# Kernel optimization log

Measured on AMD Instinct MI355X. Metric: run time of the kernel, lower is better.

The kernel has to match this reference:

```python
import jax, jax.numpy as jnp
import numpy as np

D_MODEL, D_STATE, EXPAND = 1024, 16, 2
D_INNER = D_MODEL * EXPAND
BATCH, SEQ = 4, 2048
DT = 0.1

def setup_inputs() -> dict:
    key = jax.random.key(0)
    ks = jax.random.split(key, 12)
    s = 0.02
    inp = {
        "x": jax.random.normal(ks[0], (BATCH, SEQ, D_MODEL), jnp.float32),
        "B_mod": jax.random.normal(ks[1], (BATCH, D_STATE), jnp.float32) * 0.1,
        "C_mod": jax.random.normal(ks[2], (BATCH, D_STATE), jnp.float32) * 0.1,
        "W_in": jax.random.normal(ks[3], (D_MODEL, 2 * D_INNER), jnp.float32) * s,
        "b_in": jnp.zeros((2 * D_INNER,), jnp.float32),
        "conv_w": jax.random.normal(ks[4], (D_INNER, 1, 3), jnp.float32) * 0.3,
        "conv_b": jnp.zeros((D_INNER,), jnp.float32),
        "A_log": jnp.tile(jnp.log(jnp.arange(1, D_STATE + 1, dtype=jnp.float32))[None, :], (D_INNER, 1)),
        "D": jnp.ones((D_INNER,), jnp.float32),
        "W_B": jax.random.normal(ks[5], (D_INNER, D_STATE), jnp.float32) * s,
        "b_B": jnp.zeros((D_STATE,), jnp.float32),
        "W_C": jax.random.normal(ks[6], (D_INNER, D_STATE), jnp.float32) * s,
        "b_C": jnp.zeros((D_STATE,), jnp.float32),
        "W_out": jax.random.normal(ks[7], (D_INNER, D_MODEL), jnp.float32) * s,
        "b_out": jnp.zeros((D_MODEL,), jnp.float32),
    }
    return inp

def _silu(v):
    return v * jax.nn.sigmoid(v)

def reference(x, B_mod, C_mod, W_in, b_in, conv_w, conv_b, A_log, D, W_B, b_B, W_C, b_C, W_out, b_out):
    # in_proj + split + gate
    xr = x @ W_in + b_in                      # (B, L, 2*D_INNER)
    x_ssm, x_res = jnp.split(xr, 2, axis=-1)
    x_ssm = _silu(x_ssm)
    # depthwise conv1d, kernel 3, padding 1
    xc = jnp.transpose(x_ssm, (0, 2, 1))      # (B, C, L)
    xc = jax.lax.conv_general_dilated(
        xc, conv_w, window_strides=(1,), padding=[(1, 1)],
        dimension_numbers=("NCH", "OIH", "NCH"), feature_group_count=D_INNER)
    xc = xc + conv_b[None, :, None]
    x_ssm = jnp.transpose(xc, (0, 2, 1))      # (B, L, D_INNER)
    # SSM params
    A = -jnp.exp(A_log)                       # (D_INNER, D_STATE)
    A_bar = jnp.exp(A * DT)
    B = x_ssm @ W_B + b_B + B_mod[:, None, :] # (B, L, D_STATE)
    C = x_ssm @ W_C + b_C + C_mod[:, None, :]
    # sequential scan over time
    def step(h, inp):
        xt, Bt, Ct = inp                      # (B,D_INNER), (B,S), (B,S)
        h = A_bar[None] * h + xt[:, :, None] * Bt[:, None, :]
        yt = jnp.einsum("bds,bs->bd", h, Ct)
        return h, yt
    h0 = jnp.zeros((x.shape[0], D_INNER, D_STATE), x.dtype)
    xs = (jnp.moveaxis(x_ssm, 1, 0), jnp.moveaxis(B, 1, 0), jnp.moveaxis(C, 1, 0))
    _, ys = jax.lax.scan(step, h0, xs)        # (L, B, D_INNER)
    y = jnp.moveaxis(ys, 0, 1) + D[None, None, :] * x_ssm
    y = y * _silu(x_res)
    return y @ W_out + b_out
```

## Files before the change

### kernel.cpp

```cpp
#include <hip/hip_runtime.h>
#include <stdint.h>

#define D_MODEL 1024
#define D_STATE 16
#define D_INNER 2048
#define BATCH   4
#define SEQ     2048
#define ML      (BATCH*SEQ)
#define CH      64
#define NCHUNK  (SEQ/CH)
#define KSEG    8

typedef unsigned short u16;
typedef u16   u16x8  __attribute__((ext_vector_type(8)));
typedef short s16x8  __attribute__((ext_vector_type(8)));
typedef float f32x4  __attribute__((ext_vector_type(4)));

__device__ __forceinline__ float b2f(u16 u){
  union { uint32_t i; float f; } v; v.i = ((uint32_t)u) << 16; return v.f;
}
__device__ __forceinline__ u16 f2b(float f){
  uint32_t x = __float_as_uint(f);
  return (u16)((x + 0x7fffu + ((x >> 16) & 1u)) >> 16);
}
__device__ __forceinline__ float silu_f(float v){
  return v / (1.f + __expf(-v));
}
__device__ __forceinline__ void gl_lds16(const void* gp, void* lp){
  __builtin_amdgcn_global_load_lds(
      (const __attribute__((address_space(1))) void*)gp,
      (__attribute__((address_space(3))) void*)lp, 16, 0, 0);
}

__global__ __launch_bounds__(256) void transpose_cast_k(const float* __restrict__ in,
                                                        u16* __restrict__ out,
                                                        int R, int C){
  __shared__ float tile[32][33];
  int bx = blockIdx.x * 32, by = blockIdx.y * 32;
  int tx = threadIdx.x & 31, ty = threadIdx.x >> 5;
  #pragma unroll
  for (int i = 0; i < 32; i += 8)
    tile[ty + i][tx] = in[(size_t)(by + ty + i) * C + bx + tx];
  __syncthreads();
  #pragma unroll
  for (int i = 0; i < 32; i += 8)
    out[(size_t)(bx + ty + i) * R + by + tx] = f2b(tile[tx][ty + i]);
}

__global__ __launch_bounds__(256) void cast_k(const float* __restrict__ in,
                                              u16* __restrict__ out){
  size_t i = ((size_t)blockIdx.x * 256 + threadIdx.x) * 8;
  f32x4 a = *(const f32x4*)(in + i);
  f32x4 b = *(const f32x4*)(in + i + 4);
  u16x8 o;
  #pragma unroll
  for (int j = 0; j < 4; ++j){ o[j] = f2b(a[j]); o[4+j] = f2b(b[j]); }
  *(u16x8*)(out + i) = o;
}

__global__ __launch_bounds__(256) void bc_wt_k(const float* __restrict__ W_B,
                                               const float* __restrict__ W_C,
                                               u16* __restrict__ Wt){
  int n = blockIdx.y;
  int k = blockIdx.x * 256 + threadIdx.x;
  const float* src = (n < 16) ? W_B : W_C;
  Wt[(size_t)n * D_INNER + k] = f2b(src[(size_t)k * 16 + (n & 15)]);
}

#define G1_K  1024
#define G1_NT (G1_K/64)

__global__ __launch_bounds__(512, 2) void gemm1_k(const u16* __restrict__ A,
                                                  const u16* __restrict__ Bt,
                                                  const float* __restrict__ bias,
                                                  u16* __restrict__ out0,
                                                  u16* __restrict__ out1){
  __shared__ __align__(16) u16 ldsAll[256*264];
  u16* ldsA = ldsAll;
  u16* ldsB = ldsAll + 4*8192;

  const int bid = blockIdx.x;
  const int xcd = bid & 7, t2 = bid >> 3;
  const int n0 = (xcd*2 + (t2 & 1)) * 256;
  const int m0 = (t2 >> 1) * 256;

  const int tid  = threadIdx.x;
  const int wave = tid >> 6, lane = tid & 63;
  const int wr = wave >> 2;
  const int wc = wave & 3;
  const int lrow = lane & 15;
  const int q    = lane >> 4;

  const int cx0  = ((q ^ (lrow & 7)) << 3);
  const int cx1  = cx0 ^ 32;
  const int arow = lrow * 64;

  const int srow = lane >> 3;
  const int scol = (((lane & 7) ^ (lane >> 3)) << 3);

  auto stageA = [&](int buf, int h, int k0){
    const u16* s = A + (size_t)(m0 + h*128 + wave*16 + srow) * G1_K + k0 + scol;
    u16* d = ldsA + (buf*2 + h)*8192 + wave*1024;
    gl_lds16(s,                  d);
    gl_lds16(s + (size_t)8*G1_K, d + 512);
  };
  auto stageB = [&](int buf, int h, int k0){
    const u16* s = Bt + (size_t)(n0 + h*128 + wave*16 + srow) * G1_K + k0 + scol;
    u16* d = ldsB + (buf*2 + h)*8192 + wave*1024;
    gl_lds16(s,                  d);
    gl_lds16(s + (size_t)8*G1_K, d + 512);
  };

  f32x4 acc[8][4];
  #pragma unroll
  for (int i = 0; i < 8; ++i)
    #pragma unroll
    for (int j = 0; j < 4; ++j) acc[i][j] = (f32x4){0.f,0.f,0.f,0.f};

  s16x8 aA[2][2], aB[2][2];
  s16x8 bX[4][2], bY[4][2];

  #define READ_AQ(dst, Q, nb)                                            \
    { const u16* p_ = ldsA + ((nb)*2 + wr)*8192 + (Q)*2048 + arow;       \
      dst[0][0] = *(const s16x8*)(p_ + cx0);                             \
      dst[0][1] = *(const s16x8*)(p_ + cx1);                             \
      dst[1][0] = *(const s16x8*)(p_ + 1024 + cx0);                      \
      dst[1][1] = *(const s16x8*)(p_ + 1024 + cx1); }
  #define READ_B8(dst, nb)                                               \
    { const u16* p_ = ldsB + ((nb)*2 + (wc>>1))*8192 + (wc&1)*4096 + arow; \
      _Pragma("unroll")                                                  \
      for (int nj_ = 0; nj_ < 4; ++nj_){                                 \
        dst[nj_][0] = *(const s16x8*)(p_ + nj_*1024 + cx0);              \
        dst[nj_][1] = *(const s16x8*)(p_ + nj_*1024 + cx1); } }
  #define MFMA_Q(Q, AF, BF)                                              \
    { _Pragma("unroll")                                                  \
      for (int nj_ = 0; nj_ < 4; ++nj_){                                 \
        _Pragma("unroll")                                                \
        for (int kk_ = 0; kk_ < 2; ++kk_){                               \
          acc[2*(Q)][nj_]   = __builtin_amdgcn_mfma_f32_16x16x32_bf16(AF[0][kk_], BF[nj_][kk_], acc[2*(Q)][nj_],   0,0,0); \
          acc[2*(Q)+1][nj_] = __builtin_amdgcn_mfma_f32_16x16x32_bf16(AF[1][kk_], BF[nj_][kk_], acc[2*(Q)+1][nj_], 0,0,0); } } }

  stageA(0,0,0); stageA(0,1,0); stageB(0,0,0); stageB(0,1,0);
  stageB(1,0,64); stageB(1,1,64);
  asm volatile("s_waitcnt vmcnt(4)" ::: "memory");
  __builtin_amdgcn_s_barrier();
  __builtin_amdgcn_sched_barrier(0);
  READ_B8(bX, 0);
  READ_AQ(aA, 0, 0);

  auto tile_body = [&](int tt, int buf, s16x8 (&bC)[4][2], s16x8 (&bN)[4][2]){
    const int k1 = (tt+1 < G1_NT ? tt+1 : G1_NT-1) * 64;
    const int k2 = (tt+2 < G1_NT ? tt+2 : G1_NT-1) * 64;
    const int nb = buf ^ 1;

    READ_AQ(aB, 1, buf);
    stageA(nb, 1, k1);
    stageA(nb, 0, k1);
    __builtin_amdgcn_s_barrier();
    asm volatile("s_waitcnt lgkmcnt(4)" ::: "memory");
    __builtin_amdgcn_sched_barrier(0);
    __builtin_amdgcn_s_setprio(1);
    MFMA_Q(0, aA, bC);
    __builtin_amdgcn_s_setprio(0);
    __builtin_amdgcn_s_barrier();

    READ_AQ(aA, 2, buf);
    stageB(buf, 0, k2);
    __builtin_amdgcn_s_barrier();
    asm volatile("s_waitcnt lgkmcnt(4)" ::: "memory");
    __builtin_amdgcn_sched_barrier(0);
    __builtin_amdgcn_s_setprio(1);
    MFMA_Q(1, aB, bC);
    __builtin_amdgcn_s_setprio(0);
    __builtin_amdgcn_s_barrier();

    READ_AQ(aB, 3, buf);
    stageB(buf, 1, k2);
    __builtin_amdgcn_s_barrier();
    asm volatile("s_waitcnt lgkmcnt(4)" ::: "memory");
    __builtin_amdgcn_sched_barrier(0);
    __builtin_amdgcn_s_setprio(1);
    MFMA_Q(2, aA, bC);
    __builtin_amdgcn_s_setprio(0);
    __builtin_amdgcn_s_barrier();

    asm volatile("s_waitcnt vmcnt(4)" ::: "memory");
    __builtin_amdgcn_s_barrier();
    __builtin_amdgcn_sched_barrier(0);
    READ_B8(bN, nb);
    READ_AQ(aA, 0, nb);
    asm volatile("s_waitcnt lgkmcnt(12)" ::: "memory");
    __builtin_amdgcn_sched_barrier(0);
    __builtin_amdgcn_s_setprio(1);
    MFMA_Q(3, aB, bC);
    __builtin_amdgcn_s_setprio(0);
    __builtin_amdgcn_s_barrier();
  };

  for (int tt2 = 0; tt2 < G1_NT; tt2 += 2) {
    tile_body(tt2,     0, bX, bY);
    tile_body(tt2 + 1, 1, bY, bX);
  }

  asm volatile("s_waitcnt vmcnt(0)" ::: "memory");
  __syncthreads();

  #pragma unroll
  for (int nj = 0; nj < 4; ++nj) {
    const int colg = n0 + wc*64 + nj*16 + lrow;
    const float bv = bias[colg];
    const int coll = wc*64 + nj*16 + lrow;
    #pragma unroll
    for (int mi = 0; mi < 8; ++mi) {
      #pragma unroll
      for (int r = 0; r < 4; ++r) {
        const int rowl = wr*128 + mi*16 + q*4 + r;
        ldsAll[rowl*264 + coll] = f2b(silu_f(acc[mi][nj][r] + bv));
      }
    }
  }
  __syncthreads();

  u16* op = (n0 < D_INNER) ? out0 : out1;
  const int colbase = n0 & (D_INNER - 1);
  #pragma unroll
  for (int it = 0; it < 16; ++it) {
    const int f   = it*512 + tid;
    const int row = f >> 5;
    const int ch  = f & 31;
    u16x8 v = *(const u16x8*)(ldsAll + row*264 + ch*8);
    *(u16x8*)(op + (size_t)(m0 + row)*D_INNER + colbase + ch*8) = v;
  }
  #undef READ_AQ
  #undef READ_B8
  #undef MFMA_Q
}

template<int MODE>
__global__ __launch_bounds__(256) void gemm_bt(const u16* __restrict__ A,
                                               const u16* __restrict__ Bt,
                                               const float* __restrict__ bias,
                                               u16* __restrict__ out0,
                                               u16* __restrict__ out1,
                                               float* __restrict__ outf,
                                               int M, int N, int K, int n_per_xcd){
  __shared__ __align__(16) u16 Asb[2][128*32];
  __shared__ __align__(16) u16 Bsb[2][128*32];
  const int bid = blockIdx.x;
  const int xcd = bid & 7, t2 = bid >> 3;
  const int n0 = (xcd * n_per_xcd + (t2 % n_per_xcd)) * 128;
  const int m0 = (t2 / n_per_xcd) * 128;
  const int t    = threadIdx.x;
  const int wave = t >> 6, lane = t & 63;
  const int wm   = (wave >> 1) * 64, wn = (wave & 1) * 64;
  const int lrow = lane & 15, kq = (lane >> 4) * 8;
  const int srow = lane >> 2;
  const int scol = (lane & 3) * 8;

  f32x4 acc[4][4];
  #pragma unroll
  for (int i = 0; i < 4; ++i)
    #pragma unroll
    for (int j = 0; j < 4; ++j)
      acc[i][j] = (f32x4){0.f, 0.f, 0.f, 0.f};

  auto stage = [&](int buf, int k0){
    #pragma unroll
    for (int i = 0; i < 2; ++i) {
      int R0 = (wave*2 + i) * 16;
      gl_lds16(&A [(size_t)(m0 + R0 + srow)*K + k0 + scol], &Asb[buf][R0*32]);
      gl_lds16(&Bt[(size_t)(n0 + R0 + srow)*K + k0 + scol], &Bsb[buf][R0*32]);
    }
  };

  const int KT = K >> 5;
  stage(0, 0);
  __syncthreads();
  for (int kt = 0; kt < KT; ++kt) {
    const int cur = kt & 1;
    if (kt + 1 < KT) stage(1 - cur, (kt + 1) * 32);
    s16x8 af[4], bfr[4];
    #pragma unroll
    for (int i = 0; i < 4; ++i) af[i]  = *(const s16x8*)&Asb[cur][(wm + i*16 + lrow)*32 + kq];
    #pragma unroll
    for (int j = 0; j < 4; ++j) bfr[j] = *(const s16x8*)&Bsb[cur][(wn + j*16 + lrow)*32 + kq];
    #pragma unroll
    for (int i = 0; i < 4; ++i)
      #pragma unroll
      for (int j = 0; j < 4; ++j)
        acc[i][j] = __builtin_amdgcn_mfma_f32_16x16x32_bf16(af[i], bfr[j], acc[i][j], 0, 0, 0);
    __syncthreads();
  }

  const int Nh = N >> 1;
  #pragma unroll
  for (int i = 0; i < 4; ++i) {
    #pragma unroll
    for (int j = 0; j < 4; ++j) {
      int col = n0 + wn + j*16 + lrow;
      float bv = bias[col];
      #pragma unroll
      for (int r = 0; r < 4; ++r) {
        int row = m0 + wm + i*16 + (lane >> 4)*4 + r;
        float v = acc[i][j][r] + bv;
        if (MODE == 0) {
          outf[(size_t)row * N + col] = v;
        } else {
          float s = silu_f(v);
          if (col < Nh) out0[(size_t)row * Nh + col]        = f2b(s);
          else          out1[(size_t)row * Nh + (col - Nh)] = f2b(s);
        }
      }
    }
  }
}

__global__ __launch_bounds__(256) void conv_k(const u16* __restrict__ xs,
    const float* __restrict__ conv_w, const float* __restrict__ conv_b,
    u16* __restrict__ xconv){
  int bl = blockIdx.x;
  int l = bl & (SEQ-1);
  int d = threadIdx.x * 8;
  const u16* row0 = xs + (size_t)bl * D_INNER + d;

  float f0[8], fm[8], fp[8];
  { u16x8 v = *(const u16x8*)row0;
    #pragma unroll
    for (int j = 0; j < 8; ++j) f0[j] = b2f(v[j]); }
  if (l > 0) {
    u16x8 v = *(const u16x8*)(row0 - D_INNER);
    #pragma unroll
    for (int j = 0; j < 8; ++j) fm[j] = b2f(v[j]);
  } else {
    #pragma unroll
    for (int j = 0; j < 8; ++j) fm[j] = 0.f;
  }
  if (l < SEQ-1) {
    u16x8 v = *(const u16x8*)(row0 + D_INNER);
    #pragma unroll
    for (int j = 0; j < 8; ++j) fp[j] = b2f(v[j]);
  } else {
    #pragma unroll
    for (int j = 0; j < 8; ++j) fp[j] = 0.f;
  }

  const float* wp = conv_w + (size_t)d * 3;
  float wl[24];
  #pragma unroll
  for (int q = 0; q < 6; ++q){
    f32x4 v = *(const f32x4*)(wp + q*4);
    #pragma unroll
    for (int j = 0; j < 4; ++j) wl[q*4 + j] = v[j];
  }
  float cb[8];
  { f32x4 c0 = *(const f32x4*)(conv_b + d), c1 = *(const f32x4*)(conv_b + d + 4);
    #pragma unroll
    for (int j = 0; j < 4; ++j){ cb[j] = c0[j]; cb[4+j] = c1[j]; } }

  u16x8 o;
  #pragma unroll
  for (int j = 0; j < 8; ++j)
    o[j] = f2b(wl[3*j]*fm[j] + wl[3*j+1]*f0[j] + wl[3*j+2]*fp[j] + cb[j]);
  *(u16x8*)(xconv + (size_t)bl * D_INNER + d) = o;
}

__global__ __launch_bounds__(256) void bc_gemm_k(const u16* __restrict__ xconv,
                                                 const u16* __restrict__ Wt,
                                                 float* __restrict__ partial){
  __shared__ __align__(16) u16 Asb[128*40];
  __shared__ __align__(16) u16 Wsb[32*40];
  const int kseg = blockIdx.x;
  const int m0   = blockIdx.y * 128;
  const int t    = threadIdx.x;
  const int wave = t >> 6, lane = t & 63;
  const int wm   = wave * 32;
  const int lrow = lane & 15, kq = (lane >> 4) * 8;

  f32x4 acc[2][2];
  #pragma unroll
  for (int i = 0; i < 2; ++i)
    #pragma unroll
    for (int j = 0; j < 2; ++j)
      acc[i][j] = (f32x4){0.f, 0.f, 0.f, 0.f};

  const int kbase = kseg * (D_INNER / KSEG);
  for (int ks = 0; ks < (D_INNER / KSEG); ks += 32) {
    int k0 = kbase + ks;
    #pragma unroll
    for (int i = 0; i < 2; ++i) {
      int f = (i*256 + t) * 8;
      int r = f >> 5, c = f & 31;
      *(u16x8*)&Asb[r*40 + c] = *(const u16x8*)&xconv[(size_t)(m0 + r)*D_INNER + k0 + c];
    }
    if (t < 128) {
      int f = t * 8;
      int r = f >> 5, c = f & 31;
      *(u16x8*)&Wsb[r*40 + c] = *(const u16x8*)&Wt[(size_t)r*D_INNER + k0 + c];
    }
    __syncthreads();
    s16x8 af[2], wf[2];
    #pragma unroll
    for (int i = 0; i < 2; ++i) af[i] = *(const s16x8*)&Asb[(wm + i*16 + lrow)*40 + kq];
    #pragma unroll
    for (int j = 0; j < 2; ++j) wf[j] = *(const s16x8*)&Wsb[(j*16 + lrow)*40 + kq];
    #pragma unroll
    for (int i = 0; i < 2; ++i)
      #pragma unroll
      for (int j = 0; j < 2; ++j)
        acc[i][j] = __builtin_amdgcn_mfma_f32_16x16x32_bf16(af[i], wf[j], acc[i][j], 0, 0, 0);
    __syncthreads();
  }

  #pragma unroll
  for (int i = 0; i < 2; ++i)
    #pragma unroll
    for (int j = 0; j < 2; ++j)
      #pragma unroll
      for (int r = 0; r < 4; ++r) {
        int row = m0 + wm + i*16 + (lane >> 4)*4 + r;
        int col = j*16 + lrow;
        partial[((size_t)kseg * ML + row) * 32 + col] = acc[i][j][r];
      }
}

__global__ __launch_bounds__(256) void bc_reduce_k(const float* __restrict__ partial,
    const float* __restrict__ b_B, const float* __restrict__ B_mod,
    const float* __restrict__ b_C, const float* __restrict__ C_mod,
    float* __restrict__ Bbuf, float* __restrict__ Cbuf){
  int g = blockIdx.x * 256 + threadIdx.x;
  int row = g >> 5, col = g & 31;
  int b = row >> 11;
  float s = 0.f;
  #pragma unroll
  for (int seg = 0; seg < KSEG; ++seg)
    s += partial[(size_t)seg * ML * 32 + g];
  if (col < 16) Bbuf[(size_t)row*16 + col]      = s + b_B[col]      + B_mod[b*16 + col];
  else          Cbuf[(size_t)row*16 + col - 16] = s + b_C[col - 16] + C_mod[b*16 + col - 16];
}

__global__ __launch_bounds__(256) void state_k(const u16* __restrict__ xconv,
    const float* __restrict__ Bbuf, const float* __restrict__ A_log,
    float* __restrict__ hend){
  int c = blockIdx.x, db = blockIdx.y, b = blockIdx.z;
  int d = db*256 + threadIdx.x;

  float Abar[16];
  #pragma unroll
  for (int s = 0; s < 16; ++s)
    Abar[s] = __expf(-0.1f * __expf(A_log[d*16 + s]));
  float h[16];
  #pragma unroll
  for (int s = 0; s < 16; ++s) h[s] = 0.f;

  size_t base = (size_t)b * SEQ * D_INNER + (size_t)c * CH * D_INNER + d;
  const float* Br = Bbuf + ((size_t)b * SEQ + (size_t)c * CH) * 16;

  float Bc[16];
  #pragma unroll
  for (int s = 0; s < 16; ++s) Bc[s] = Br[s];
  float xn = b2f(xconv[base]);

  for (int l = 0; l < CH; ++l){
    float x = xn;
    float Bl[16];
    #pragma unroll
    for (int s = 0; s < 16; ++s) Bl[s] = Bc[s];
    if (l < CH-1){
      xn = b2f(xconv[base + (size_t)(l+1)*D_INNER]);
      #pragma unroll
      for (int s = 0; s < 16; ++s) Bc[s] = Br[(l+1)*16 + s];
    }
    #pragma unroll
    for (int s = 0; s < 16; ++s)
      h[s] = Abar[s]*h[s] + x*Bl[s];
  }
  float* hp = hend + (((size_t)(b*NCHUNK + c))*D_INNER + d)*16;
  #pragma unroll
  for (int q = 0; q < 4; ++q)
    *(f32x4*)(hp + q*4) = (f32x4){h[q*4], h[q*4+1], h[q*4+2], h[q*4+3]};
}

__global__ __launch_bounds__(256) void prefix_k(const float* __restrict__ hend,
    const float* __restrict__ A_log, float* __restrict__ hin){
  int g = blockIdx.x*256 + threadIdx.x;
  int s = g & 15;
  int d = (g >> 4) & (D_INNER-1);
  int b = g >> 15;
  float decay = __expf(-0.1f * (float)CH * __expf(A_log[d*16 + s]));
  size_t stride = (size_t)D_INNER * 16;
  const float* he = hend + (size_t)b*NCHUNK*stride + (size_t)d*16 + s;
  float*       hi = hin  + (size_t)b*NCHUNK*stride + (size_t)d*16 + s;
  float h = 0.f;
  for (int c0 = 0; c0 < NCHUNK; c0 += 8){
    float v[8];
    #pragma unroll
    for (int i = 0; i < 8; ++i) v[i] = he[(size_t)(c0+i)*stride];
    #pragma unroll
    for (int i = 0; i < 8; ++i){
      hi[(size_t)(c0+i)*stride] = h;
      h = decay*h + v[i];
    }
  }
}

__global__ __launch_bounds__(256) void scan2_k(const u16* __restrict__ xconv,
    const u16* __restrict__ gate, const float* __restrict__ Bbuf, const float* __restrict__ Cbuf,
    const float* __restrict__ A_log, const float* __restrict__ Dp,
    const float* __restrict__ hin, u16* __restrict__ ybuf){
  int c = blockIdx.x, db = blockIdx.y, b = blockIdx.z;
  int d = db*256 + threadIdx.x;

  float Abar[16];
  #pragma unroll
  for (int s = 0; s < 16; ++s)
    Abar[s] = __expf(-0.1f * __expf(A_log[d*16 + s]));
  float h[16];
  const float* hp = hin + (((size_t)(b*NCHUNK + c))*D_INNER + d)*16;
  #pragma unroll
  for (int q = 0; q < 4; ++q){
    f32x4 v = *(const f32x4*)(hp + q*4);
    #pragma unroll
    for (int j = 0; j < 4; ++j) h[q*4 + j] = v[j];
  }
  float Dd = Dp[d];

  size_t base = (size_t)b * SEQ * D_INNER + (size_t)c * CH * D_INNER + d;
  const float* Br = Bbuf + ((size_t)b * SEQ + (size_t)c * CH) * 16;
  const float* Cr = Cbuf + ((size_t)b * SEQ + (size_t)c * CH) * 16;

  float Bc[16], Cc[16];
  #pragma unroll
  for (int s = 0; s < 16; ++s){ Bc[s] = Br[s]; Cc[s] = Cr[s]; }
  float xn = b2f(xconv[base]);
  float gn = b2f(gate[base]);

  for (int l = 0; l < CH; ++l){
    float x = xn, g = gn;
    float Bl[16], Cl[16];
    #pragma unroll
    for (int s = 0; s < 16; ++s){ Bl[s] = Bc[s]; Cl[s] = Cc[s]; }
    if (l < CH-1){
      size_t idx = base + (size_t)(l+1)*D_INNER;
      xn = b2f(xconv[idx]); gn = b2f(gate[idx]);
      #pragma unroll
      for (int s = 0; s < 16; ++s){ Bc[s] = Br[(l+1)*16 + s]; Cc[s] = Cr[(l+1)*16 + s]; }
    }
    float ya[4] = {0.f, 0.f, 0.f, 0.f};
    #pragma unroll
    for (int s = 0; s < 16; ++s){
      float hv = Abar[s]*h[s] + x*Bl[s];
      h[s] = hv;
      ya[s & 3] += hv * Cl[s];
    }
    float y = ((ya[0]+ya[1]) + (ya[2]+ya[3]) + Dd*x) * g;
    ybuf[base + (size_t)l*D_INNER] = f2b(y);
  }
}

extern "C" void kernel_launch(void* const* d_in, const int* in_sizes, int n_in,
                              void* d_out, int out_size, void* d_ws, size_t ws_size,
                              hipStream_t stream){
  const float* x      = (const float*)d_in[0];
  const float* B_mod  = (const float*)d_in[1];
  const float* C_mod  = (const float*)d_in[2];
  const float* W_in   = (const float*)d_in[3];
  const float* b_in   = (const float*)d_in[4];
  const float* conv_w = (const float*)d_in[5];
  const float* conv_b = (const float*)d_in[6];
  const float* A_log  = (const float*)d_in[7];
  const float* Dp     = (const float*)d_in[8];
  const float* W_B    = (const float*)d_in[9];
  const float* b_B    = (const float*)d_in[10];
  const float* W_C    = (const float*)d_in[11];
  const float* b_C    = (const float*)d_in[12];
  const float* W_out  = (const float*)d_in[13];
  const float* b_out  = (const float*)d_in[14];
  float* out = (float*)d_out;

  char* ws = (char*)d_ws;
  size_t off = 0;
  auto alloc = [&](size_t bytes)->char* {
    char* p = ws + off; off += (bytes + 255) & ~(size_t)255; return p;
  };
  u16* Wt_in  = (u16*)alloc((size_t)(2*D_INNER)*D_MODEL*2);
  u16* Wt_out = (u16*)alloc((size_t)D_MODEL*D_INNER*2);
  u16* xs     = (u16*)alloc((size_t)ML*D_INNER*2);
  u16* gatep  = (u16*)alloc((size_t)ML*D_INNER*2);
  u16* xconv  = (u16*)alloc((size_t)ML*D_INNER*2);
  float* Bbuf = (float*)alloc((size_t)ML*D_STATE*4);
  float* Cbuf = (float*)alloc((size_t)ML*D_STATE*4);
  u16* xbf    = (u16*)alloc((size_t)ML*D_MODEL*2);
  float* hin  = (float*)alloc((size_t)BATCH*NCHUNK*D_INNER*16*4);
  u16* Wt_bc  = (u16*)alloc((size_t)32*D_INNER*2);
  float* hend    = (float*)xbf;
  float* partial = (float*)Wt_in;
  u16* ybuf = xs;

  transpose_cast_k<<<dim3((2*D_INNER)/32, D_MODEL/32), 256, 0, stream>>>(W_in, Wt_in, D_MODEL, 2*D_INNER);
  transpose_cast_k<<<dim3(D_MODEL/32, D_INNER/32),     256, 0, stream>>>(W_out, Wt_out, D_INNER, D_MODEL);
  cast_k<<<dim3((ML*D_MODEL)/(256*8)), 256, 0, stream>>>(x, xbf);
  bc_wt_k<<<dim3(D_INNER/256, 32), 256, 0, stream>>>(W_B, W_C, Wt_bc);

  gemm1_k<<<dim3(512), 512, 0, stream>>>(xbf, Wt_in, b_in, xs, gatep);

  conv_k<<<dim3(ML), 256, 0, stream>>>(xs, conv_w, conv_b, xconv);

  bc_gemm_k<<<dim3(KSEG, ML/128), 256, 0, stream>>>(xconv, Wt_bc, partial);
  bc_reduce_k<<<dim3((ML*32)/256), 256, 0, stream>>>(
      partial, b_B, B_mod, b_C, C_mod, Bbuf, Cbuf);

  state_k<<<dim3(NCHUNK, D_INNER/256, BATCH), 256, 0, stream>>>(xconv, Bbuf, A_log, hend);
  prefix_k<<<dim3((BATCH*D_INNER*16)/256), 256, 0, stream>>>(hend, A_log, hin);
  scan2_k<<<dim3(NCHUNK, D_INNER/256, BATCH), 256, 0, stream>>>(
      xconv, gatep, Bbuf, Cbuf, A_log, Dp, hin, ybuf);

  gemm_bt<0><<<dim3(512), 256, 0, stream>>>(
      ybuf, Wt_out, b_out, nullptr, nullptr, out, ML, D_MODEL, D_INNER, 1);
}
```

Measured before the change: 354.9 us.

## Fuse depthwise conv into BC GEMM and scan kernels, drop conv kernel

Removes the standalone conv kernel and its bf16 intermediate buffer. The 3-tap depthwise convolution is now recomputed inside the BC projection GEMM, via a shared-memory halo tile, and inside both chunked scan kernels, via a rolling three-element register window. This avoids writing and re-reading a full activation-sized tensor, at the cost of redundant conv arithmetic and an extra shared-memory stage plus barrier in the GEMM. ybuf gets its own allocation because xs is now still read by the scan.

New measurement: 368.8 us. +3.9%, slower.

```diff
diff --git a/kernel.cpp b/kernel.cpp
--- a/kernel.cpp
+++ b/kernel.cpp
@@ -315,58 +315,12 @@
   }
 }
 
-__global__ __launch_bounds__(256) void conv_k(const u16* __restrict__ xs,
-    const float* __restrict__ conv_w, const float* __restrict__ conv_b,
-    u16* __restrict__ xconv){
-  int bl = blockIdx.x;
-  int l = bl & (SEQ-1);
-  int d = threadIdx.x * 8;
-  const u16* row0 = xs + (size_t)bl * D_INNER + d;
-
-  float f0[8], fm[8], fp[8];
-  { u16x8 v = *(const u16x8*)row0;
-    #pragma unroll
-    for (int j = 0; j < 8; ++j) f0[j] = b2f(v[j]); }
-  if (l > 0) {
-    u16x8 v = *(const u16x8*)(row0 - D_INNER);
-    #pragma unroll
-    for (int j = 0; j < 8; ++j) fm[j] = b2f(v[j]);
-  } else {
-    #pragma unroll
-    for (int j = 0; j < 8; ++j) fm[j] = 0.f;
-  }
-  if (l < SEQ-1) {
-    u16x8 v = *(const u16x8*)(row0 + D_INNER);
-    #pragma unroll
-    for (int j = 0; j < 8; ++j) fp[j] = b2f(v[j]);
-  } else {
-    #pragma unroll
-    for (int j = 0; j < 8; ++j) fp[j] = 0.f;
-  }
-
-  const float* wp = conv_w + (size_t)d * 3;
-  float wl[24];
-  #pragma unroll
-  for (int q = 0; q < 6; ++q){
-    f32x4 v = *(const f32x4*)(wp + q*4);
-    #pragma unroll
-    for (int j = 0; j < 4; ++j) wl[q*4 + j] = v[j];
-  }
-  float cb[8];
-  { f32x4 c0 = *(const f32x4*)(conv_b + d), c1 = *(const f32x4*)(conv_b + d + 4);
-    #pragma unroll
-    for (int j = 0; j < 4; ++j){ cb[j] = c0[j]; cb[4+j] = c1[j]; } }
-
-  u16x8 o;
-  #pragma unroll
-  for (int j = 0; j < 8; ++j)
-    o[j] = f2b(wl[3*j]*fm[j] + wl[3*j+1]*f0[j] + wl[3*j+2]*fp[j] + cb[j]);
-  *(u16x8*)(xconv + (size_t)bl * D_INNER + d) = o;
-}
-
-__global__ __launch_bounds__(256) void bc_gemm_k(const u16* __restrict__ xconv,
+__global__ __launch_bounds__(256) void bc_gemm_k(const u16* __restrict__ xs,
+                                                 const float* __restrict__ conv_w,
+                                                 const float* __restrict__ conv_b,
                                                  const u16* __restrict__ Wt,
                                                  float* __restrict__ partial){
+  __shared__ __align__(16) u16 Rsb[130*40];
   __shared__ __align__(16) u16 Asb[128*40];
   __shared__ __align__(16) u16 Wsb[32*40];
   const int kseg = blockIdx.x;
@@ -375,6 +329,9 @@
   const int wave = t >> 6, lane = t & 63;
   const int wm   = wave * 32;
   const int lrow = lane & 15, kq = (lane >> 4) * 8;
+  const bool zfirst = (m0 & (SEQ-1)) == 0;
+  const bool zlast  = ((m0+128) & (SEQ-1)) == 0;
+  const int ccol = t & 31, r0c = (t >> 5) * 16;
 
   f32x4 acc[2][2];
   #pragma unroll
@@ -386,16 +343,36 @@
   const int kbase = kseg * (D_INNER / KSEG);
   for (int ks = 0; ks < (D_INNER / KSEG); ks += 32) {
     int k0 = kbase + ks;
-    #pragma unroll
-    for (int i = 0; i < 2; ++i) {
-      int f = (i*256 + t) * 8;
-      int r = f >> 5, c = f & 31;
-      *(u16x8*)&Asb[r*40 + c] = *(const u16x8*)&xconv[(size_t)(m0 + r)*D_INNER + k0 + c];
-    }
     if (t < 128) {
       int f = t * 8;
       int r = f >> 5, c = f & 31;
       *(u16x8*)&Wsb[r*40 + c] = *(const u16x8*)&Wt[(size_t)r*D_INNER + k0 + c];
+    }
+    #pragma unroll
+    for (int i = 0; i < 3; ++i) {
+      int idx = i*256 + t;
+      if (idx < 520) {
+        int r = idx >> 2, c = (idx & 3) * 8;
+        u16x8 v = (u16x8){0,0,0,0,0,0,0,0};
+        bool zero = (r == 0 && zfirst) || (r == 129 && zlast);
+        if (!zero)
+          v = *(const u16x8*)&xs[(size_t)(m0 - 1 + r)*D_INNER + k0 + c];
+        *(u16x8*)&Rsb[r*40 + c] = v;
+      }
+    }
+    __syncthreads();
+    {
+      const int dcol = k0 + ccol;
+      const float cw0 = conv_w[dcol*3], cw1 = conv_w[dcol*3+1], cw2 = conv_w[dcol*3+2];
+      const float cbv = conv_b[dcol];
+      #pragma unroll
+      for (int r = 0; r < 16; ++r) {
+        int rr = r0c + r;
+        float v = cw0 * b2f(Rsb[rr*40 + ccol])
+                + cw1 * b2f(Rsb[(rr+1)*40 + ccol])
+                + cw2 * b2f(Rsb[(rr+2)*40 + ccol]) + cbv;
+        Asb[rr*40 + ccol] = f2b(v);
+      }
     }
     __syncthreads();
     s16x8 af[2], wf[2];
@@ -438,7 +415,8 @@
   else          Cbuf[(size_t)row*16 + col - 16] = s + b_C[col - 16] + C_mod[b*16 + col - 16];
 }
 
-__global__ __launch_bounds__(256) void state_k(const u16* __restrict__ xconv,
+__global__ __launch_bounds__(256) void state_k(const u16* __restrict__ xs,
+    const float* __restrict__ conv_w, const float* __restrict__ conv_b,
     const float* __restrict__ Bbuf, const float* __restrict__ A_log,
     float* __restrict__ hend){
   int c = blockIdx.x, db = blockIdx.y, b = blockIdx.z;
@@ -452,27 +430,33 @@
   #pragma unroll
   for (int s = 0; s < 16; ++s) h[s] = 0.f;
 
+  const float w0 = conv_w[d*3], w1 = conv_w[d*3+1], w2 = conv_w[d*3+2], cb = conv_b[d];
   size_t base = (size_t)b * SEQ * D_INNER + (size_t)c * CH * D_INNER + d;
   const float* Br = Bbuf + ((size_t)b * SEQ + (size_t)c * CH) * 16;
-
+  const int l0 = c * CH;
+
+  float xm = (l0 > 0) ? b2f(xs[base - D_INNER]) : 0.f;
+  float x0 = b2f(xs[base]);
+  float xp = b2f(xs[base + D_INNER]);
   float Bc[16];
   #pragma unroll
   for (int s = 0; s < 16; ++s) Bc[s] = Br[s];
-  float xn = b2f(xconv[base]);
 
   for (int l = 0; l < CH; ++l){
-    float x = xn;
+    float xq = 0.f;
+    if (l0 + l + 2 < SEQ) xq = b2f(xs[base + (size_t)(l+2)*D_INNER]);
     float Bl[16];
     #pragma unroll
     for (int s = 0; s < 16; ++s) Bl[s] = Bc[s];
     if (l < CH-1){
-      xn = b2f(xconv[base + (size_t)(l+1)*D_INNER]);
       #pragma unroll
       for (int s = 0; s < 16; ++s) Bc[s] = Br[(l+1)*16 + s];
     }
+    float xc = w0*xm + w1*x0 + w2*xp + cb;
     #pragma unroll
     for (int s = 0; s < 16; ++s)
-      h[s] = Abar[s]*h[s] + x*Bl[s];
+      h[s] = Abar[s]*h[s] + xc*Bl[s];
+    xm = x0; x0 = xp; xp = xq;
   }
   float* hp = hend + (((size_t)(b*NCHUNK + c))*D_INNER + d)*16;
   #pragma unroll
@@ -503,8 +487,10 @@
   }
 }
 
-__global__ __launch_bounds__(256) void scan2_k(const u16* __restrict__ xconv,
-    const u16* __restrict__ gate, const float* __restrict__ Bbuf, const float* __restrict__ Cbuf,
+__global__ __launch_bounds__(256) void scan2_k(const u16* __restrict__ xs,
+    const u16* __restrict__ gate,
+    const float* __restrict__ conv_w, const float* __restrict__ conv_b,
+    const float* __restrict__ Bbuf, const float* __restrict__ Cbuf,
     const float* __restrict__ A_log, const float* __restrict__ Dp,
     const float* __restrict__ hin, u16* __restrict__ ybuf){
   int c = blockIdx.x, db = blockIdx.y, b = blockIdx.z;
@@ -523,37 +509,43 @@
     for (int j = 0; j < 4; ++j) h[q*4 + j] = v[j];
   }
   float Dd = Dp[d];
+  const float w0 = conv_w[d*3], w1 = conv_w[d*3+1], w2 = conv_w[d*3+2], cb = conv_b[d];
 
   size_t base = (size_t)b * SEQ * D_INNER + (size_t)c * CH * D_INNER + d;
   const float* Br = Bbuf + ((size_t)b * SEQ + (size_t)c * CH) * 16;
   const float* Cr = Cbuf + ((size_t)b * SEQ + (size_t)c * CH) * 16;
-
+  const int l0 = c * CH;
+
+  float xm = (l0 > 0) ? b2f(xs[base - D_INNER]) : 0.f;
+  float x0 = b2f(xs[base]);
+  float xp = b2f(xs[base + D_INNER]);
   float Bc[16], Cc[16];
   #pragma unroll
   for (int s = 0; s < 16; ++s){ Bc[s] = Br[s]; Cc[s] = Cr[s]; }
-  float xn = b2f(xconv[base]);
-  float gn = b2f(gate[base]);
+  float gcur = b2f(gate[base]);
 
   for (int l = 0; l < CH; ++l){
-    float x = xn, g = gn;
+    float xq = 0.f;
+    if (l0 + l + 2 < SEQ) xq = b2f(xs[base + (size_t)(l+2)*D_INNER]);
+    float gnext = (l < CH-1) ? b2f(gate[base + (size_t)(l+1)*D_INNER]) : 0.f;
     float Bl[16], Cl[16];
     #pragma unroll
     for (int s = 0; s < 16; ++s){ Bl[s] = Bc[s]; Cl[s] = Cc[s]; }
     if (l < CH-1){
-      size_t idx = base + (size_t)(l+1)*D_INNER;
-      xn = b2f(xconv[idx]); gn = b2f(gate[idx]);
       #pragma unroll
       for (int s = 0; s < 16; ++s){ Bc[s] = Br[(l+1)*16 + s]; Cc[s] = Cr[(l+1)*16 + s]; }
     }
+    float xc = w0*xm + w1*x0 + w2*xp + cb;
     float ya[4] = {0.f, 0.f, 0.f, 0.f};
     #pragma unroll
     for (int s = 0; s < 16; ++s){
-      float hv = Abar[s]*h[s] + x*Bl[s];
+      float hv = Abar[s]*h[s] + xc*Bl[s];
       h[s] = hv;
       ya[s & 3] += hv * Cl[s];
     }
-    float y = ((ya[0]+ya[1]) + (ya[2]+ya[3]) + Dd*x) * g;
+    float y = ((ya[0]+ya[1]) + (ya[2]+ya[3]) + Dd*xc) * gcur;
     ybuf[base + (size_t)l*D_INNER] = f2b(y);
+    xm = x0; x0 = xp; xp = xq; gcur = gnext;
   }
 }
 
@@ -586,7 +578,7 @@
   u16* Wt_out = (u16*)alloc((size_t)D_MODEL*D_INNER*2);
   u16* xs     = (u16*)alloc((size_t)ML*D_INNER*2);
   u16* gatep  = (u16*)alloc((size_t)ML*D_INNER*2);
-  u16* xconv  = (u16*)alloc((size_t)ML*D_INNER*2);
+  u16* ybuf   = (u16*)alloc((size_t)ML*D_INNER*2);
   float* Bbuf = (float*)alloc((size_t)ML*D_STATE*4);
   float* Cbuf = (float*)alloc((size_t)ML*D_STATE*4);
   u16* xbf    = (u16*)alloc((size_t)ML*D_MODEL*2);
@@ -594,7 +586,6 @@
   u16* Wt_bc  = (u16*)alloc((size_t)32*D_INNER*2);
   float* hend    = (float*)xbf;
   float* partial = (float*)Wt_in;
-  u16* ybuf = xs;
 
   transpose_cast_k<<<dim3((2*D_INNER)/32, D_MODEL/32), 256, 0, stream>>>(W_in, Wt_in, D_MODEL, 2*D_INNER);
   transpose_cast_k<<<dim3(D_MODEL/32, D_INNER/32),     256, 0, stream>>>(W_out, Wt_out, D_INNER, D_MODEL);
@@ -603,16 +594,15 @@
 
   gemm1_k<<<dim3(512), 512, 0, stream>>>(xbf, Wt_in, b_in, xs, gatep);
 
-  conv_k<<<dim3(ML), 256, 0, stream>>>(xs, conv_w, conv_b, xconv);
-
-  bc_gemm_k<<<dim3(KSEG, ML/128), 256, 0, stream>>>(xconv, Wt_bc, partial);
+  bc_gemm_k<<<dim3(KSEG, ML/128), 256, 0, stream>>>(xs, conv_w, conv_b, Wt_bc, partial);
   bc_reduce_k<<<dim3((ML*32)/256), 256, 0, stream>>>(
       partial, b_B, B_mod, b_C, C_mod, Bbuf, Cbuf);
 
-  state_k<<<dim3(NCHUNK, D_INNER/256, BATCH), 256, 0, stream>>>(xconv, Bbuf, A_log, hend);
+  state_k<<<dim3(NCHUNK, D_INNER/256, BATCH), 256, 0, stream>>>(
+      xs, conv_w, conv_b, Bbuf, A_log, hend);
   prefix_k<<<dim3((BATCH*D_INNER*16)/256), 256, 0, stream>>>(hend, A_log, hin);
   scan2_k<<<dim3(NCHUNK, D_INNER/256, BATCH), 256, 0, stream>>>(
-      xconv, gatep, Bbuf, Cbuf, A_log, Dp, hin, ybuf);
+      xs, gatep, conv_w, conv_b, Bbuf, Cbuf, A_log, Dp, hin, ybuf);
 
   gemm_bt<0><<<dim3(512), 256, 0, stream>>>(
       ybuf, Wt_out, b_out, nullptr, nullptr, out, ML, D_MODEL, D_INNER, 1);
```
